# Performance work log

Measured on AMD Instinct MI355X. Metric: run time of the kernel, lower is better.

Reference implementation:

```python
import jax, jax.numpy as jnp
import numpy as np

D = 131072  # inner feature dim
N = 84      # 4*(1 + 4*(1 + 4)) entries emitted by calc_probs


def calc_probs(logits):
    # softmax over the 4 logits, then emit, in original nested-loop order:
    # for i: p_i, then for j: p_i*p_j followed by p_i*p_j*p_k for k in 0..3
    p = jax.nn.softmax(logits)                      # (4,)
    pairs = p[:, None] * p[None, :]                 # (4,4)
    triples = pairs[:, :, None] * p[None, None, :]  # (4,4,4)
    inner = jnp.concatenate([pairs[:, :, None], triples], axis=2)  # (4,4,5)
    full = jnp.concatenate([p[:, None], inner.reshape(4, 20)], axis=1)  # (4,21)
    return full.reshape(N)  # (84,)


def setup_inputs() -> dict:
    key = jax.random.key(0)
    ks = jax.random.split(key, 6)
    return {
        "BEV": jax.random.normal(ks[0], (1,), dtype=jnp.float32),
        "ST0": jax.random.normal(ks[1], (N, D), dtype=jnp.float32),
        "Weight0": jax.random.normal(ks[2], (N, D, 1), dtype=jnp.float32),
        "ST1": jax.random.normal(ks[3], (N, D), dtype=jnp.float32),
        "Weight1": jax.random.normal(ks[4], (N, D, 1), dtype=jnp.float32),
        "Problem": 1,
        "probs0": jnp.array([2.0327, 1.0198, 1.024, 0.9935], dtype=jnp.float32),
        "probs1": jnp.array([2.6661, 1.0168, 1.02, 0.9971], dtype=jnp.float32),
        "probs2": jnp.array([2.8173, 1.016, 1.0189, 0.9978], dtype=jnp.float32),
        "probs3": jnp.array([2.9183, 1.0154, 1.0181, 0.9981], dtype=jnp.float32),
        "probs4": jnp.array([2.9689, 1.0151, 1.0177, 0.9983], dtype=jnp.float32),
        "pBEV": jnp.array([0.1822], dtype=jnp.float32),
        "pB": jnp.array([3.1475], dtype=jnp.float32),
    }


def reference(BEV, ST0, Weight0, ST1, Weight1, Problem,
              probs0, probs1, probs2, probs3, probs4, pBEV, pB):
    p0 = calc_probs(probs0)
    p1 = calc_probs(probs1)
    p2 = calc_probs(probs2)
    p3 = calc_probs(probs3)
    p4 = calc_probs(probs4)
    # fused sigmoid + per-row dot, replacing the Python loop over 84 rows
    bev = pBEV * BEV  # (1,)
    tmp0 = jnp.einsum('id,id->i', jax.nn.sigmoid(pB * (bev + ST0)), Weight0[..., 0])  # (84,)
    tmp1 = jnp.einsum('id,id->i', jax.nn.sigmoid(pB * (bev + ST1)), Weight1[..., 0])  # (84,)
    vals = jnp.stack([p0 @ tmp0, p1 @ tmp1, p2 @ tmp1, p3 @ tmp1, p4 @ tmp1])
    return jnp.mean(vals)
```

## Files before the change

kernel.cpp:

```cpp
#include <hip/hip_runtime.h>
#include <hip/hip_bf16.h>


#define D_DIM   131072
#define N_ROWS  84
#define CHUNKS  32
#define CHUNK   (D_DIM / CHUNKS)

__device__ inline float prob_entry(const float* __restrict__ logits, int t) {
    float l0 = logits[0], l1 = logits[1], l2 = logits[2], l3 = logits[3];
    float m  = fmaxf(fmaxf(l0, l1), fmaxf(l2, l3));
    float e0 = __expf(l0 - m), e1 = __expf(l1 - m);
    float e2 = __expf(l2 - m), e3 = __expf(l3 - m);
    float inv = 1.0f / (e0 + e1 + e2 + e3);
    float p[4] = {e0 * inv, e1 * inv, e2 * inv, e3 * inv};
    int i = t / 21;
    int r = t - i * 21;
    if (r == 0) return p[i];
    r -= 1;
    int j = r / 5;
    int s = r - j * 5;
    float v = p[i] * p[j];
    return (s == 0) ? v : v * p[s - 1];
}

__global__ __launch_bounds__(256) void probsnet_kernel(
    const float* __restrict__ BEV,
    const float* __restrict__ ST0, const float* __restrict__ W0,
    const float* __restrict__ ST1, const float* __restrict__ W1,
    const float* __restrict__ probs0, const float* __restrict__ probs1,
    const float* __restrict__ probs2, const float* __restrict__ probs3,
    const float* __restrict__ probs4,
    const float* __restrict__ pBEV, const float* __restrict__ pB,
    float* __restrict__ out)
{
    const int bid    = blockIdx.x;
    const int tensor = bid / (N_ROWS * CHUNKS);
    const int rem    = bid - tensor * (N_ROWS * CHUNKS);
    const int row    = rem / CHUNKS;
    const int chunk  = rem - row * CHUNKS;

    const float bev = pBEV[0] * BEV[0];
    const float pb  = pB[0];

    const size_t base = (size_t)row * D_DIM + (size_t)chunk * CHUNK;
    const float* __restrict__ st = (tensor == 0 ? ST0 : ST1) + base;
    const float* __restrict__ wp = (tensor == 0 ? W0  : W1 ) + base;

    const int t = threadIdx.x;

    float4 s[4], w[4];
    #pragma unroll
    for (int j = 0; j < 4; ++j) {
        const int idx = (j * 256 + t) * 4;
        s[j] = *(const float4*)(st + idx);
    }
    #pragma unroll
    for (int j = 0; j < 4; ++j) {
        const int idx = (j * 256 + t) * 4;
        w[j] = *(const float4*)(wp + idx);
    }

    float acc = 0.0f;
    #pragma unroll
    for (int j = 0; j < 4; ++j) {
        float sg;
        sg = 1.0f / (1.0f + __expf(-pb * (bev + s[j].x))); acc += sg * w[j].x;
        sg = 1.0f / (1.0f + __expf(-pb * (bev + s[j].y))); acc += sg * w[j].y;
        sg = 1.0f / (1.0f + __expf(-pb * (bev + s[j].z))); acc += sg * w[j].z;
        sg = 1.0f / (1.0f + __expf(-pb * (bev + s[j].w))); acc += sg * w[j].w;
    }

    #pragma unroll
    for (int off = 32; off > 0; off >>= 1)
        acc += __shfl_down(acc, off, 64);

    __shared__ float red[4];
    const int wave = threadIdx.x >> 6;
    const int lane = threadIdx.x & 63;
    if (lane == 0) red[wave] = acc;
    __syncthreads();

    if (threadIdx.x == 0) {
        float bs = red[0] + red[1] + red[2] + red[3];
        float pw;
        if (tensor == 0) {
            pw = prob_entry(probs0, row);
        } else {
            pw = prob_entry(probs1, row) + prob_entry(probs2, row)
               + prob_entry(probs3, row) + prob_entry(probs4, row);
        }
        atomicAdd(out, bs * pw * 0.2f);
    }
}

extern "C" void kernel_launch(void* const* d_in, const int* in_sizes, int n_in,
                              void* d_out, int out_size, void* d_ws, size_t ws_size,
                              hipStream_t stream) {
    const float* BEV    = (const float*)d_in[0];
    const float* ST0    = (const float*)d_in[1];
    const float* W0     = (const float*)d_in[2];
    const float* ST1    = (const float*)d_in[3];
    const float* W1     = (const float*)d_in[4];
    const float* probs0 = (const float*)d_in[6];
    const float* probs1 = (const float*)d_in[7];
    const float* probs2 = (const float*)d_in[8];
    const float* probs3 = (const float*)d_in[9];
    const float* probs4 = (const float*)d_in[10];
    const float* pBEV   = (const float*)d_in[11];
    const float* pB     = (const float*)d_in[12];
    float* out = (float*)d_out;

    hipMemsetAsync(out, 0, sizeof(float), stream);

    const int grid = 2 * N_ROWS * CHUNKS;
    probsnet_kernel<<<grid, 256, 0, stream>>>(
        BEV, ST0, W0, ST1, W1,
        probs0, probs1, probs2, probs3, probs4,
        pBEV, pB, out);
}
```

Before: 223.6 us.

## Flatten work into persistent-ish blocks with prefetch loop and two-pass reduction

Replaces the 5376 one-shot blocks with 1792 blocks that each stream 12 float4 pairs per thread through a 4-deep register prefetch ring. Per-row probability weights are computed once per block into shared memory and applied per element. The global atomicAdd and memset are replaced by per-block partials in workspace plus a second single-block reduction kernel. This cuts per-block launch and atomic overhead and adds memory-level parallelism, at the cost of a second kernel launch and a workspace dependency.

After: 202.4 us. -9.5%, faster.

```diff
diff --git a/kernel.cpp b/kernel.cpp
--- a/kernel.cpp
+++ b/kernel.cpp
@@ -2,10 +2,14 @@
 #include <hip/hip_bf16.h>
 
 
-#define D_DIM   131072
-#define N_ROWS  84
-#define CHUNKS  32
-#define CHUNK   (D_DIM / CHUNKS)
+#define D_DIM      131072
+#define N_ROWS     84
+#define ROW_F4     (D_DIM / 4)
+#define TENSOR_F4  (N_ROWS * ROW_F4)
+#define BLOCKS     1792
+#define T0_BLOCKS  896
+#define F4_PER_BLOCK 3072
+#define F4_PER_THREAD 12
 
 __device__ inline float prob_entry(const float* __restrict__ logits, int t) {
     float l0 = logits[0], l1 = logits[1], l2 = logits[2], l3 = logits[3];
@@ -24,7 +28,7 @@
     return (s == 0) ? v : v * p[s - 1];
 }
 
-__global__ __launch_bounds__(256) void probsnet_kernel(
+__global__ __launch_bounds__(256, 4) void probsnet_main(
     const float* __restrict__ BEV,
     const float* __restrict__ ST0, const float* __restrict__ W0,
     const float* __restrict__ ST1, const float* __restrict__ W1,
@@ -32,43 +36,53 @@
     const float* __restrict__ probs2, const float* __restrict__ probs3,
     const float* __restrict__ probs4,
     const float* __restrict__ pBEV, const float* __restrict__ pB,
-    float* __restrict__ out)
+    float* __restrict__ partials)
 {
     const int bid    = blockIdx.x;
-    const int tensor = bid / (N_ROWS * CHUNKS);
-    const int rem    = bid - tensor * (N_ROWS * CHUNKS);
-    const int row    = rem / CHUNKS;
-    const int chunk  = rem - row * CHUNKS;
+    const int t      = threadIdx.x;
+    const int tensor = (bid >= T0_BLOCKS) ? 1 : 0;
+    const int fb     = bid * F4_PER_BLOCK - tensor * TENSOR_F4;
 
     const float bev = pBEV[0] * BEV[0];
     const float pb  = pB[0];
 
-    const size_t base = (size_t)row * D_DIM + (size_t)chunk * CHUNK;
-    const float* __restrict__ st = (tensor == 0 ? ST0 : ST1) + base;
-    const float* __restrict__ wp = (tensor == 0 ? W0  : W1 ) + base;
+    __shared__ float wrow[N_ROWS];
+    if (t < N_ROWS) {
+        wrow[t] = (tensor == 0)
+            ? prob_entry(probs0, t)
+            : prob_entry(probs1, t) + prob_entry(probs2, t)
+            + prob_entry(probs3, t) + prob_entry(probs4, t);
+    }
+    __syncthreads();
 
-    const int t = threadIdx.x;
+    const float4* __restrict__ stp =
+        (const float4*)(tensor ? ST1 : ST0) + fb + t;
+    const float4* __restrict__ wpp =
+        (const float4*)(tensor ? W1 : W0) + fb + t;
 
-    float4 s[4], w[4];
+    float4 sb[4], wb[4];
     #pragma unroll
-    for (int j = 0; j < 4; ++j) {
-        const int idx = (j * 256 + t) * 4;
-        s[j] = *(const float4*)(st + idx);
-    }
-    #pragma unroll
-    for (int j = 0; j < 4; ++j) {
-        const int idx = (j * 256 + t) * 4;
-        w[j] = *(const float4*)(wp + idx);
+    for (int k = 0; k < 4; ++k) {
+        sb[k] = stp[k * 256];
+        wb[k] = wpp[k * 256];
     }
 
     float acc = 0.0f;
     #pragma unroll
-    for (int j = 0; j < 4; ++j) {
-        float sg;
-        sg = 1.0f / (1.0f + __expf(-pb * (bev + s[j].x))); acc += sg * w[j].x;
-        sg = 1.0f / (1.0f + __expf(-pb * (bev + s[j].y))); acc += sg * w[j].y;
-        sg = 1.0f / (1.0f + __expf(-pb * (bev + s[j].z))); acc += sg * w[j].z;
-        sg = 1.0f / (1.0f + __expf(-pb * (bev + s[j].w))); acc += sg * w[j].w;
+    for (int k = 0; k < F4_PER_THREAD; ++k) {
+        float4 s4 = sb[k & 3];
+        float4 w4 = wb[k & 3];
+        if (k + 4 < F4_PER_THREAD) {
+            sb[k & 3] = stp[(k + 4) * 256];
+            wb[k & 3] = wpp[(k + 4) * 256];
+        }
+        float sum;
+        sum  = w4.x / (1.0f + __expf(-pb * (bev + s4.x)));
+        sum += w4.y / (1.0f + __expf(-pb * (bev + s4.y)));
+        sum += w4.z / (1.0f + __expf(-pb * (bev + s4.z)));
+        sum += w4.w / (1.0f + __expf(-pb * (bev + s4.w)));
+        const int row = (fb + t + k * 256) >> 15;
+        acc = fmaf(wrow[row], sum, acc);
     }
 
     #pragma unroll
@@ -76,22 +90,36 @@
         acc += __shfl_down(acc, off, 64);
 
     __shared__ float red[4];
-    const int wave = threadIdx.x >> 6;
-    const int lane = threadIdx.x & 63;
+    const int wave = t >> 6;
+    const int lane = t & 63;
     if (lane == 0) red[wave] = acc;
     __syncthreads();
 
-    if (threadIdx.x == 0) {
-        float bs = red[0] + red[1] + red[2] + red[3];
-        float pw;
-        if (tensor == 0) {
-            pw = prob_entry(probs0, row);
-        } else {
-            pw = prob_entry(probs1, row) + prob_entry(probs2, row)
-               + prob_entry(probs3, row) + prob_entry(probs4, row);
-        }
-        atomicAdd(out, bs * pw * 0.2f);
-    }
+    if (t == 0)
+        partials[bid] = red[0] + red[1] + red[2] + red[3];
+}
+
+__global__ __launch_bounds__(256) void probsnet_reduce(
+    const float* __restrict__ partials, float* __restrict__ out)
+{
+    const int t = threadIdx.x;
+    float acc = 0.0f;
+    #pragma unroll
+    for (int k = 0; k < BLOCKS / 256; ++k)
+        acc += partials[t + k * 256];
+
+    #pragma unroll
+    for (int off = 32; off > 0; off >>= 1)
+        acc += __shfl_down(acc, off, 64);
+
+    __shared__ float red[4];
+    const int wave = t >> 6;
+    const int lane = t & 63;
+    if (lane == 0) red[wave] = acc;
+    __syncthreads();
+
+    if (t == 0)
+        out[0] = (red[0] + red[1] + red[2] + red[3]) * 0.2f;
 }
 
 extern "C" void kernel_launch(void* const* d_in, const int* in_sizes, int n_in,
@@ -109,13 +137,14 @@
     const float* probs4 = (const float*)d_in[10];
     const float* pBEV   = (const float*)d_in[11];
     const float* pB     = (const float*)d_in[12];
-    float* out = (float*)d_out;
 
-    hipMemsetAsync(out, 0, sizeof(float), stream);
+    float* partials = (float*)d_ws;
+    float* out      = (float*)d_out;
 
-    const int grid = 2 * N_ROWS * CHUNKS;
-    probsnet_kernel<<<grid, 256, 0, stream>>>(
+    probsnet_main<<<BLOCKS, 256, 0, stream>>>(
         BEV, ST0, W0, ST1, W1,
         probs0, probs1, probs2, probs3, probs4,
-        pBEV, pB, out);
+        pBEV, pB, partials);
+
+    probsnet_reduce<<<1, 256, 0, stream>>>(partials, out);
 }
```
